# Optimization experiments

Hardware: AMD Instinct MI355X
Metric: run time of the kernel (lower is better)

## Reference

```python
import jax, jax.numpy as jnp
import numpy as np

C_IN, C_OUT, K, H, W = 16, 16, 3, 1024, 1024
PAD = 1  # 'same' padding for 3x3 stride-1


def setup_inputs() -> dict:
    key = jax.random.key(0)
    kx, kw, kb = jax.random.split(key, 3)
    x = jax.random.normal(kx, (1, C_IN, H, W), dtype=jnp.float32)
    weight = jax.random.normal(kw, (C_OUT, C_IN, K, K), dtype=jnp.float32) * 0.05
    bias = jax.random.normal(kb, (C_OUT,), dtype=jnp.float32) * 0.05
    return {"x": x, "weight": weight, "bias": bias}


def reference(x, weight, bias):
    # Original module: im2col (unfold) + matmul + reshape + bias add.
    # Mathematically identical to a dense 2D convolution (cross-correlation),
    # expressed here as the fused implicit-GEMM conv primitive.
    out = jax.lax.conv_general_dilated(
        x, weight,
        window_strides=(1, 1),
        padding=((PAD, PAD), (PAD, PAD)),
        dimension_numbers=("NCHW", "OIHW", "NCHW"),
    )  # [1, C_OUT, H, W]
    # out_unf.view(*output_shape) drops the batch dim (batch must be 1)
    return out[0] + bias[:, None, None]
```

## Files before the change

kernel.cpp:

```cpp
#include <hip/hip_runtime.h>


#define HH 1024
#define WW 1024
#define CIN 16
#define COUT 16
#define TW 64
#define TH 16
#define LROWS (TH + 2)
#define LCOLS (TW + 2)
#define PIX 16
#define XPW 1026

typedef short v8s __attribute__((ext_vector_type(8)));
typedef float v4f __attribute__((ext_vector_type(4)));
typedef unsigned int u32;

__device__ __forceinline__ unsigned short f32_bf16(float f) {
    union { float f; u32 u; } v;
    v.f = f;
    u32 u = v.u;
    u += 0x7fffu + ((u >> 16) & 1u);
    return (unsigned short)(u >> 16);
}

__global__ __launch_bounds__(256)
void conv_pack(const float* __restrict__ x, unsigned short* __restrict__ xp) {
    const int hp = blockIdx.x;
    const int h = hp - 1;
    if ((unsigned)h >= (unsigned)HH) {
        uint4 z = {0u, 0u, 0u, 0u};
        uint4* dst = (uint4*)(xp + (size_t)hp * XPW * PIX);
        for (int i = threadIdx.x; i < XPW * 2; i += 256) dst[i] = z;
        return;
    }
    if (threadIdx.x < 4) {
        uint4 z = {0u, 0u, 0u, 0u};
        if (threadIdx.x < 2) {
            uint4* d0 = (uint4*)(xp + (size_t)hp * XPW * PIX);
            d0[threadIdx.x] = z;
        } else {
            uint4* d1 = (uint4*)(xp + ((size_t)hp * XPW + 1025) * PIX);
            d1[threadIdx.x - 2] = z;
        }
    }
    const int t = threadIdx.x;
    for (int wbase = 0; wbase < WW; wbase += 512) {
        const int w = wbase + 2 * t;
        const float* src = x + (size_t)h * WW + w;
        u32 p0[8], p1[8];
        #pragma unroll
        for (int c = 0; c < CIN; c += 2) {
            float2 va = *(const float2*)(src + (size_t)c * HH * WW);
            float2 vb = *(const float2*)(src + (size_t)(c + 1) * HH * WW);
            p0[c >> 1] = (u32)f32_bf16(va.x) | ((u32)f32_bf16(vb.x) << 16);
            p1[c >> 1] = (u32)f32_bf16(va.y) | ((u32)f32_bf16(vb.y) << 16);
        }
        uint4* dst = (uint4*)(xp + ((size_t)hp * XPW + (w + 1)) * PIX);
        dst[0] = *(uint4*)&p0[0];
        dst[1] = *(uint4*)&p0[4];
        dst[2] = *(uint4*)&p1[0];
        dst[3] = *(uint4*)&p1[4];
    }
}


typedef const __attribute__((address_space(1))) u32* gptr_t;
typedef __attribute__((address_space(3))) u32* lptr_t;

__global__ __launch_bounds__(256, 4)
void conv3x3_mfma(const unsigned short* __restrict__ xp,
                  const float* __restrict__ wgt,
                  const float* __restrict__ bias,
                  float* __restrict__ out) {
    __shared__ __align__(16) unsigned short sm[LROWS * LCOLS * PIX];

    const int tid = threadIdx.x;
    const int lane = tid & 63;
    const int wave = tid >> 6;
    const int h0 = blockIdx.y * TH;
    const int w0 = blockIdx.x * TW;

    const unsigned char* xpb = (const unsigned char*)xp;
    #pragma unroll
    for (int it = 0; it < 10; ++it) {
        int cid = it * 256 + wave * 64 + lane;
        if (cid < (LROWS * LCOLS * PIX * 2) / 16) {
            int r = cid / 132;
            int o = cid - r * 132;
            const unsigned char* g =
                xpb + ((size_t)(h0 + r) * XPW + w0) * (PIX * 2) + (size_t)o * 16;
            lptr_t l = (lptr_t)((__attribute__((address_space(3))) unsigned char*)sm +
                                (it * 256 + wave * 64) * 16);
            __builtin_amdgcn_global_load_lds((gptr_t)g, l, 16, 0, 0);
        }
    }

    const int m = lane & 15;
    const int q = lane >> 4;
    const int qh = q >> 1;
    const int qc = (q & 1) * 8;

    v8s a1[3], a2[3];
    for (int kw = 0; kw < 3; ++kw) {
        for (int j = 0; j < 8; ++j) {
            a1[kw][j] = (short)f32_bf16(wgt[((m * CIN + (qc + j)) * 3 + qh) * 3 + kw]);
            short t2 = 0;
            if (q < 2)
                t2 = (short)f32_bf16(wgt[((m * CIN + (q * 8 + j)) * 3 + 2) * 3 + kw]);
            a2[kw][j] = t2;
        }
    }
    float bl[4];
    #pragma unroll
    for (int i = 0; i < 4; ++i) bl[i] = bias[q * 4 + i];

    __syncthreads();

    const int colbase = wave * 16 + m;
    for (int r = 0; r < TH; ++r) {
        v4f accA = {0.f, 0.f, 0.f, 0.f};
        v4f accB = {0.f, 0.f, 0.f, 0.f};
        #pragma unroll
        for (int kw = 0; kw < 3; ++kw) {
            const int col = colbase + kw;
            v8s b1 = *(const v8s*)&sm[((r + qh) * LCOLS + col) * PIX + qc];
            accA = __builtin_amdgcn_mfma_f32_16x16x32_bf16(a1[kw], b1, accA, 0, 0, 0);
            v8s b2 = {0, 0, 0, 0, 0, 0, 0, 0};
            if (q < 2)
                b2 = *(const v8s*)&sm[((r + 2) * LCOLS + col) * PIX + q * 8];
            accB = __builtin_amdgcn_mfma_f32_16x16x32_bf16(a2[kw], b2, accB, 0, 0, 0);
        }
        const int h = h0 + r;
        float* op = out + (size_t)h * WW + (w0 + colbase);
        #pragma unroll
        for (int i = 0; i < 4; ++i)
            op[(size_t)(q * 4 + i) * (HH * WW)] = accA[i] + accB[i] + bl[i];
    }
}

__global__ __launch_bounds__(256, 4)
void conv3x3_mfma_fb(const float* __restrict__ x,
                     const float* __restrict__ wgt,
                     const float* __restrict__ bias,
                     float* __restrict__ out) {
    __shared__ __align__(16) unsigned short sm[LROWS * LCOLS * PIX];
    const int tid = threadIdx.x;
    const int h0 = blockIdx.y * TH;
    const int w0 = blockIdx.x * TW;
    const int E = LROWS * LCOLS * CIN;
    for (int e = tid; e < E; e += 256) {
        int c = e % LCOLS;
        int t = e / LCOLS;
        int r = t % LROWS;
        int cin = t / LROWS;
        int gh = h0 - 1 + r;
        int gw = w0 - 1 + c;
        float v = 0.0f;
        if ((unsigned)gh < (unsigned)HH && (unsigned)gw < (unsigned)WW)
            v = x[cin * (HH * WW) + gh * WW + gw];
        sm[(r * LCOLS + c) * PIX + cin] = f32_bf16(v);
    }
    const int lane = tid & 63;
    const int wave = tid >> 6;
    const int m = lane & 15;
    const int q = lane >> 4;
    const int qh = q >> 1;
    const int qc = (q & 1) * 8;
    v8s a1[3], a2[3];
    for (int kw = 0; kw < 3; ++kw) {
        for (int j = 0; j < 8; ++j) {
            a1[kw][j] = (short)f32_bf16(wgt[((m * CIN + (qc + j)) * 3 + qh) * 3 + kw]);
            short t2 = 0;
            if (q < 2)
                t2 = (short)f32_bf16(wgt[((m * CIN + (q * 8 + j)) * 3 + 2) * 3 + kw]);
            a2[kw][j] = t2;
        }
    }
    float bl[4];
    #pragma unroll
    for (int i = 0; i < 4; ++i) bl[i] = bias[q * 4 + i];
    __syncthreads();
    const int colbase = wave * 16 + m;
    for (int r = 0; r < TH; ++r) {
        v4f accA = {0.f, 0.f, 0.f, 0.f};
        v4f accB = {0.f, 0.f, 0.f, 0.f};
        #pragma unroll
        for (int kw = 0; kw < 3; ++kw) {
            const int col = colbase + kw;
            v8s b1 = *(const v8s*)&sm[((r + qh) * LCOLS + col) * PIX + qc];
            accA = __builtin_amdgcn_mfma_f32_16x16x32_bf16(a1[kw], b1, accA, 0, 0, 0);
            v8s b2 = {0, 0, 0, 0, 0, 0, 0, 0};
            if (q < 2)
                b2 = *(const v8s*)&sm[((r + 2) * LCOLS + col) * PIX + q * 8];
            accB = __builtin_amdgcn_mfma_f32_16x16x32_bf16(a2[kw], b2, accB, 0, 0, 0);
        }
        const int h = h0 + r;
        float* op = out + h * WW + (w0 + colbase);
        #pragma unroll
        for (int i = 0; i < 4; ++i)
            op[(q * 4 + i) * (HH * WW)] = accA[i] + accB[i] + bl[i];
    }
}

extern "C" void kernel_launch(void* const* d_in, const int* in_sizes, int n_in,
                              void* d_out, int out_size, void* d_ws, size_t ws_size,
                              hipStream_t stream) {
    const float* x = (const float*)d_in[0];
    const float* w = (const float*)d_in[1];
    const float* b = (const float*)d_in[2];
    float* out = (float*)d_out;
    const size_t need = (size_t)XPW * XPW * PIX * sizeof(unsigned short);
    if (ws_size >= need) {
        unsigned short* xp = (unsigned short*)d_ws;
        conv_pack<<<dim3(XPW), dim3(256), 0, stream>>>(x, xp);
        dim3 grid(WW / TW, HH / TH);
        conv3x3_mfma<<<grid, dim3(256), 0, stream>>>(xp, w, b, out);
    } else {
        dim3 grid(WW / TW, HH / TH);
        conv3x3_mfma_fb<<<grid, dim3(256), 0, stream>>>(x, w, b, out);
    }
}
```

Before: 149.2 us.

## Repack conv K dimension into five MFMAs with XOR-swizzled LDS layout

Restructures the implicit-GEMM reduction so the 144-wide K (9 taps × 16 channels) is packed into 5 bf16 MFMAs of K=32 instead of 6, with only the last one partially zero-padded. Each lane gets a per-group LDS offset for its tap and channel half. The LDS staging now XOR-swizzles 16-byte chunks to reduce bank conflicts on the B-operand reads, and the row loop is unrolled by 4. It also drops the second accumulator and its extra add. The risk is more index arithmetic per load and possible conflicts from the new access pattern.

```diff
diff --git a/kernel.cpp b/kernel.cpp
--- a/kernel.cpp
+++ b/kernel.cpp
@@ -11,6 +11,7 @@
 #define LCOLS (TW + 2)
 #define PIX 16
 #define XPW 1026
+#define NCHUNK (LROWS * LCOLS * 2)
 
 typedef short v8s __attribute__((ext_vector_type(8)));
 typedef float v4f __attribute__((ext_vector_type(4)));
@@ -64,7 +65,6 @@
     }
 }
 
-
 typedef const __attribute__((address_space(1))) u32* gptr_t;
 typedef __attribute__((address_space(3))) u32* lptr_t;
 
@@ -84,10 +84,11 @@
     const unsigned char* xpb = (const unsigned char*)xp;
     #pragma unroll
     for (int it = 0; it < 10; ++it) {
-        int cid = it * 256 + wave * 64 + lane;
-        if (cid < (LROWS * LCOLS * PIX * 2) / 16) {
-            int r = cid / 132;
-            int o = cid - r * 132;
+        int P = it * 256 + wave * 64 + lane;
+        if (P < NCHUNK) {
+            int L = P ^ ((P >> 3) & 1);
+            int r = L / 132;
+            int o = L - r * 132;
             const unsigned char* g =
                 xpb + ((size_t)(h0 + r) * XPW + w0) * (PIX * 2) + (size_t)o * 16;
             lptr_t l = (lptr_t)((__attribute__((address_space(3))) unsigned char*)sm +
@@ -98,17 +99,24 @@
 
     const int m = lane & 15;
     const int q = lane >> 4;
-    const int qh = q >> 1;
-    const int qc = (q & 1) * 8;
-
-    v8s a1[3], a2[3];
-    for (int kw = 0; kw < 3; ++kw) {
+    const int colbase = wave * 16 + m;
+
+    v8s a[5];
+    int Kofs[5];
+    #pragma unroll
+    for (int g5 = 0; g5 < 5; ++g5) {
+        int t = 4 * g5 + q;
+        int tt = t > 17 ? 17 : t;
+        int khkw = tt >> 1;
+        int kh = khkw / 3;
+        int kw = khkw - 3 * kh;
+        int half = tt & 1;
+        Kofs[g5] = (kh * LCOLS + colbase + kw) * 2 + half;
+        bool valid = t < 18;
+        #pragma unroll
         for (int j = 0; j < 8; ++j) {
-            a1[kw][j] = (short)f32_bf16(wgt[((m * CIN + (qc + j)) * 3 + qh) * 3 + kw]);
-            short t2 = 0;
-            if (q < 2)
-                t2 = (short)f32_bf16(wgt[((m * CIN + (q * 8 + j)) * 3 + 2) * 3 + kw]);
-            a2[kw][j] = t2;
+            float wv = valid ? wgt[((m * CIN + half * 8 + j) * 3 + kh) * 3 + kw] : 0.0f;
+            a[g5][j] = (short)f32_bf16(wv);
         }
     }
     float bl[4];
@@ -117,25 +125,20 @@
 
     __syncthreads();
 
-    const int colbase = wave * 16 + m;
+    #pragma unroll 4
     for (int r = 0; r < TH; ++r) {
-        v4f accA = {0.f, 0.f, 0.f, 0.f};
-        v4f accB = {0.f, 0.f, 0.f, 0.f};
-        #pragma unroll
-        for (int kw = 0; kw < 3; ++kw) {
-            const int col = colbase + kw;
-            v8s b1 = *(const v8s*)&sm[((r + qh) * LCOLS + col) * PIX + qc];
-            accA = __builtin_amdgcn_mfma_f32_16x16x32_bf16(a1[kw], b1, accA, 0, 0, 0);
-            v8s b2 = {0, 0, 0, 0, 0, 0, 0, 0};
-            if (q < 2)
-                b2 = *(const v8s*)&sm[((r + 2) * LCOLS + col) * PIX + q * 8];
-            accB = __builtin_amdgcn_mfma_f32_16x16x32_bf16(a2[kw], b2, accB, 0, 0, 0);
-        }
-        const int h = h0 + r;
-        float* op = out + (size_t)h * WW + (w0 + colbase);
+        v4f acc = {0.f, 0.f, 0.f, 0.f};
+        #pragma unroll
+        for (int g5 = 0; g5 < 5; ++g5) {
+            int c = r * 132 + Kofs[g5];
+            int phys = c ^ ((c >> 3) & 1);
+            v8s b = *(const v8s*)(sm + phys * 8);
+            acc = __builtin_amdgcn_mfma_f32_16x16x32_bf16(a[g5], b, acc, 0, 0, 0);
+        }
+        float* op = out + (size_t)(h0 + r) * WW + (w0 + colbase);
         #pragma unroll
         for (int i = 0; i < 4; ++i)
-            op[(size_t)(q * 4 + i) * (HH * WW)] = accA[i] + accB[i] + bl[i];
+            op[(size_t)(q * 4 + i) * (HH * WW)] = acc[i] + bl[i];
     }
 }
 
```

Result: faster. 145.1 us (-2.8%).
